# Kernel tuning notes

Hardware: AMD Instinct MI355X
Metric: run time of the kernel (lower is better)

## Reference

```python
import jax, jax.numpy as jnp
import numpy as np

V, L, D, C = 50000, 512, 300, 128
KS = (3, 4, 5)
B = 64


def setup_inputs() -> dict:
    key = jax.random.key(0)
    ks = jax.random.split(key, 12)
    inp = {
        "x": jax.random.randint(ks[0], (B, L), 0, V),
        "embed_w": jax.random.normal(ks[1], (V, D), jnp.float32) * 0.1,
        "conv_w": jax.random.normal(ks[2], (C, D), jnp.float32) * 0.05,
        "conv_b": jax.random.normal(ks[3], (C,), jnp.float32) * 0.05,
        "fc3_w": jax.random.normal(ks[4], (L - 3,), jnp.float32) * 0.04,
        "fc3_b": jax.random.normal(ks[5], (1,), jnp.float32) * 0.04,
        "fc4_w": jax.random.normal(ks[6], (L - 4,), jnp.float32) * 0.04,
        "fc4_b": jax.random.normal(ks[7], (1,), jnp.float32) * 0.04,
        "fc5_w": jax.random.normal(ks[8], (L - 5,), jnp.float32) * 0.04,
        "fc5_b": jax.random.normal(ks[9], (1,), jnp.float32) * 0.04,
        "fc_w": jax.random.normal(ks[10], (C, C * len(KS)), jnp.float32) * 0.05,
        "fc_b": jax.random.normal(ks[11], (C,), jnp.float32) * 0.05,
    }
    return inp


def reference(x, embed_w, conv_w, conv_b, fc3_w, fc3_b, fc4_w, fc4_b,
              fc5_w, fc5_b, fc_w, fc_b):
    # Embedding lookup: [B, L, D]
    emb = embed_w[x]
    # Exclusive prefix sum over the sequence dim (O(L) sliding sums).
    cs = jnp.concatenate(
        [jnp.zeros_like(emb[:, :1]), jnp.cumsum(emb, axis=1)], axis=1)  # [B, L+1, D]
    fcs = ((fc3_w, fc3_b), (fc4_w, fc4_b), (fc5_w, fc5_b))
    outs = []
    for k, (wk, bk) in zip(KS, fcs):
        # Window i sums tokens i..i+k-1; only L-k windows (range(L-k) in original).
        win = cs[:, k:L] - cs[:, :L - k]                      # [B, L-k, D]
        # conv_sim: dot each window-sum against C label vectors (kernel (1, D)).
        sim = jnp.einsum('bld,cd->bcl', win, conv_w) + conv_b[None, :, None]
        # Dropout is identity in eval; fcs[k]: Linear(L-k, 1) shared across channels.
        outs.append(jnp.einsum('bcl,l->bc', sim, wk) + bk)    # [B, C]
    h = jnp.concatenate(outs, axis=1)                          # [B, C*3]
    return h @ fc_w.T + fc_b                                   # [B, C]
```

## Files before the change

kernel.cpp:

```cpp
#include <hip/hip_runtime.h>
#include <stdint.h>

#define BB 64
#define LL 512
#define DD 300
#define CC 128

#define OFF_GRED (BB * 32 * 3 * DD)
#define OFF_HT   (OFF_GRED + BB * 3 * DD)
#define OFF_SKBK (OFF_HT + BB * 3 * CC)

__global__ __launch_bounds__(256) void k_gather(
    const int* __restrict__ x, const float* __restrict__ embed,
    const float* __restrict__ w3, const float* __restrict__ w4,
    const float* __restrict__ w5, float* __restrict__ Gpart) {
  const int b = blockIdx.x >> 4;
  const int tc = blockIdx.x & 15;
  const int tid = threadIdx.x;
  const int sub = tid >> 7;
  const int stid = tid & 127;

  __shared__ int sx[32];
  __shared__ float su[3][32];

  if (tid < 32) {
    const int t = tc * 32 + tid;
    sx[tid] = x[b * LL + t];
    const float* ws[3] = {w3, w4, w5};
#pragma unroll
    for (int kk = 0; kk < 3; ++kk) {
      const int k = kk + 3;
      int lo = t - k + 1; if (lo < 0) lo = 0;
      int hi = t; const int lim = LL - k - 1; if (hi > lim) hi = lim;
      float s = 0.f;
      for (int l = lo; l <= hi; ++l) s += ws[kk][l];
      su[kk][tid] = s;
    }
  }
  __syncthreads();

  float a0x = 0.f, a0y = 0.f, a1x = 0.f, a1y = 0.f, a2x = 0.f, a2y = 0.f;
  float c0x = 0.f, c0y = 0.f, c1x = 0.f, c1y = 0.f, c2x = 0.f, c2y = 0.f;
  const bool tail = stid < (DD / 2 - 128);

#pragma unroll
  for (int half = 0; half < 2; ++half) {
    const int base = sub * 16 + half * 8;
    float2 v[8], u[8];
#pragma unroll
    for (int i = 0; i < 8; ++i) {
      const float2* rp = (const float2*)(embed + (size_t)sx[base + i] * DD);
      v[i] = rp[stid];
    }
    if (tail) {
#pragma unroll
      for (int i = 0; i < 8; ++i) {
        const float2* rp = (const float2*)(embed + (size_t)sx[base + i] * DD);
        u[i] = rp[128 + stid];
      }
    }
#pragma unroll
    for (int i = 0; i < 8; ++i) {
      const int j = base + i;
      const float w0 = su[0][j], w1 = su[1][j], w2 = su[2][j];
      a0x += w0 * v[i].x; a0y += w0 * v[i].y;
      a1x += w1 * v[i].x; a1y += w1 * v[i].y;
      a2x += w2 * v[i].x; a2y += w2 * v[i].y;
      if (tail) {
        c0x += w0 * u[i].x; c0y += w0 * u[i].y;
        c1x += w1 * u[i].x; c1y += w1 * u[i].y;
        c2x += w2 * u[i].x; c2y += w2 * u[i].y;
      }
    }
  }

  const int p = tc * 2 + sub;
  float* Gp = Gpart + (size_t)(b * 32 + p) * (3 * DD);
  const int d0 = 2 * stid;
  Gp[0 * DD + d0] = a0x; Gp[0 * DD + d0 + 1] = a0y;
  Gp[1 * DD + d0] = a1x; Gp[1 * DD + d0 + 1] = a1y;
  Gp[2 * DD + d0] = a2x; Gp[2 * DD + d0 + 1] = a2y;
  if (tail) {
    const int d1 = 2 * (128 + stid);
    Gp[0 * DD + d1] = c0x; Gp[0 * DD + d1 + 1] = c0y;
    Gp[1 * DD + d1] = c1x; Gp[1 * DD + d1 + 1] = c1y;
    Gp[2 * DD + d1] = c2x; Gp[2 * DD + d1 + 1] = c2y;
  }
}

__global__ __launch_bounds__(256) void k_reduce(
    const float* __restrict__ Gpart,
    const float* __restrict__ w3, const float* __restrict__ b3,
    const float* __restrict__ w4, const float* __restrict__ b4,
    const float* __restrict__ w5, const float* __restrict__ b5,
    float* __restrict__ Gred, float* __restrict__ skbk) {
  const int blk = blockIdx.x;
  const int tid = threadIdx.x;

  if (blk < 225) {
    const int gid = blk * 256 + tid;
    const int out = gid >> 2;
    const int r = gid & 3;
    const int b = out / 225;
    const int q = out - b * 225;
    const float4* gp =
        (const float4*)Gpart + (size_t)b * 32 * 225 + (size_t)r * 8 * 225 + q;
    float4 s = gp[0];
#pragma unroll
    for (int p = 1; p < 8; ++p) {
      const float4 v = gp[(size_t)p * 225];
      s.x += v.x; s.y += v.y; s.z += v.z; s.w += v.w;
    }
#pragma unroll
    for (int off = 1; off <= 2; off <<= 1) {
      s.x += __shfl_down(s.x, off, 64);
      s.y += __shfl_down(s.y, off, 64);
      s.z += __shfl_down(s.z, off, 64);
      s.w += __shfl_down(s.w, off, 64);
    }
    if (r == 0) ((float4*)Gred)[out] = s;
  } else {
    __shared__ float red[256];
    const int kk = blk - 225;
    const float* wk = (kk == 0) ? w3 : ((kk == 1) ? w4 : w5);
    const float* bk = (kk == 0) ? b3 : ((kk == 1) ? b4 : b5);
    const int len = LL - (kk + 3);
    float s = (tid < len) ? wk[tid] : 0.f;
    if (tid + 256 < len) s += wk[tid + 256];
    red[tid] = s;
    __syncthreads();
    for (int off = 128; off >= 1; off >>= 1) {
      if (tid < off) red[tid] += red[tid + off];
      __syncthreads();
    }
    if (tid == 0) { skbk[kk] = red[0]; skbk[3 + kk] = bk[0]; }
  }
}

__global__ __launch_bounds__(256) void k_sim(
    const float* __restrict__ Gred, const float* __restrict__ conv_w,
    const float* __restrict__ conv_b, const float* __restrict__ skbk,
    float* __restrict__ hT) {
  const int o = blockIdx.x * 4 + (threadIdx.x >> 6);
  const int lane = threadIdx.x & 63;
  const int b = o / 384;
  const int j = o - b * 384;
  const int kk = j >> 7;
  const int cp = j & 127;

  const float2* cwp = (const float2*)(conv_w + cp * DD);
  const float2* g2 = (const float2*)(Gred + (b * 3 + kk) * DD);

  float acc;
  {
    const float2 v = cwp[lane];
    const float2 g = g2[lane];
    acc = v.x * g.x + v.y * g.y;
  }
  {
    const float2 v = cwp[lane + 64];
    const float2 g = g2[lane + 64];
    acc += v.x * g.x + v.y * g.y;
  }
  if (lane < 22) {
    const float2 v = cwp[lane + 128];
    const float2 g = g2[lane + 128];
    acc += v.x * g.x + v.y * g.y;
  }
#pragma unroll
  for (int off = 32; off >= 1; off >>= 1) acc += __shfl_down(acc, off, 64);
  if (lane == 0) {
    hT[b * (3 * CC) + j] = acc + conv_b[cp] * skbk[kk] + skbk[3 + kk];
  }
}

__global__ __launch_bounds__(256) void k_fc(
    const float* __restrict__ hT, const float* __restrict__ fcw,
    const float* __restrict__ fcb, float* __restrict__ out) {
  const int o = blockIdx.x * 4 + (threadIdx.x >> 6);
  const int lane = threadIdx.x & 63;
  const int b = o >> 7;
  const int c = o & 127;

  const float* fr = fcw + c * (3 * CC);
  const float* hr = hT + b * (3 * CC);
  float acc = 0.f;
#pragma unroll
  for (int s = 0; s < 6; ++s) acc += fr[s * 64 + lane] * hr[s * 64 + lane];
#pragma unroll
  for (int off = 32; off >= 1; off >>= 1) acc += __shfl_down(acc, off, 64);
  if (lane == 0) out[b * CC + c] = acc + fcb[c];
}

extern "C" void kernel_launch(void* const* d_in, const int* in_sizes, int n_in,
                              void* d_out, int out_size, void* d_ws,
                              size_t ws_size, hipStream_t stream) {
  const int* x = (const int*)d_in[0];
  const float* embed = (const float*)d_in[1];
  const float* conv_w = (const float*)d_in[2];
  const float* conv_b = (const float*)d_in[3];
  const float* fc3w = (const float*)d_in[4];
  const float* fc3b = (const float*)d_in[5];
  const float* fc4w = (const float*)d_in[6];
  const float* fc4b = (const float*)d_in[7];
  const float* fc5w = (const float*)d_in[8];
  const float* fc5b = (const float*)d_in[9];
  const float* fcw = (const float*)d_in[10];
  const float* fcb = (const float*)d_in[11];

  float* Gpart = (float*)d_ws;
  float* Gred = (float*)d_ws + OFF_GRED;
  float* hT = (float*)d_ws + OFF_HT;
  float* skbk = (float*)d_ws + OFF_SKBK;

  k_gather<<<dim3(BB * 16), dim3(256), 0, stream>>>(x, embed, fc3w, fc4w,
                                                    fc5w, Gpart);
  k_reduce<<<dim3(228), dim3(256), 0, stream>>>(Gpart, fc3w, fc3b, fc4w, fc4b,
                                                fc5w, fc5b, Gred, skbk);
  k_sim<<<dim3(6144), dim3(256), 0, stream>>>(Gred, conv_w, conv_b, skbk, hT);
  k_fc<<<dim3(2048), dim3(256), 0, stream>>>(hT, fcw, fcb, (float*)d_out);
}
```

Baseline: 129.7 us.

## Fuse partial-sum reduction and conv similarity into one kernel per batch-kernel pair

Merges the Gpart reduction, the fc weight-sum reduction and the conv_w dot-product stage into one kernel launched with one block per (batch, window size). Each block reduces its 32 partials into shared memory, computes the weight sum locally, and then loops over the 128 conv channels with one wavefront per 32 channels. This removes a kernel launch and the Gred/skbk global round trip. In exchange the grid drops to 192 blocks, and the weight-sum reduction is recomputed in every block.

```diff
diff --git a/kernel.cpp b/kernel.cpp
--- a/kernel.cpp
+++ b/kernel.cpp
@@ -6,9 +6,7 @@
 #define DD 300
 #define CC 128
 
-#define OFF_GRED (BB * 32 * 3 * DD)
-#define OFF_HT   (OFF_GRED + BB * 3 * DD)
-#define OFF_SKBK (OFF_HT + BB * 3 * CC)
+#define OFF_HT (BB * 32 * 3 * DD)
 
 __global__ __launch_bounds__(256) void k_gather(
     const int* __restrict__ x, const float* __restrict__ embed,
@@ -88,89 +86,91 @@
   }
 }
 
-__global__ __launch_bounds__(256) void k_reduce(
-    const float* __restrict__ Gpart,
+__global__ __launch_bounds__(256) void k_redsim(
+    const float* __restrict__ Gpart, const float* __restrict__ conv_w,
+    const float* __restrict__ conv_b,
     const float* __restrict__ w3, const float* __restrict__ b3,
     const float* __restrict__ w4, const float* __restrict__ b4,
     const float* __restrict__ w5, const float* __restrict__ b5,
-    float* __restrict__ Gred, float* __restrict__ skbk) {
+    float* __restrict__ hT) {
   const int blk = blockIdx.x;
+  const int b = blk / 3;
+  const int kk = blk - b * 3;
   const int tid = threadIdx.x;
-
-  if (blk < 225) {
-    const int gid = blk * 256 + tid;
-    const int out = gid >> 2;
-    const int r = gid & 3;
-    const int b = out / 225;
-    const int q = out - b * 225;
-    const float4* gp =
-        (const float4*)Gpart + (size_t)b * 32 * 225 + (size_t)r * 8 * 225 + q;
-    float4 s = gp[0];
-#pragma unroll
-    for (int p = 1; p < 8; ++p) {
-      const float4 v = gp[(size_t)p * 225];
-      s.x += v.x; s.y += v.y; s.z += v.z; s.w += v.w;
-    }
-#pragma unroll
-    for (int off = 1; off <= 2; off <<= 1) {
-      s.x += __shfl_down(s.x, off, 64);
-      s.y += __shfl_down(s.y, off, 64);
-      s.z += __shfl_down(s.z, off, 64);
-      s.w += __shfl_down(s.w, off, 64);
-    }
-    if (r == 0) ((float4*)Gred)[out] = s;
-  } else {
-    __shared__ float red[256];
-    const int kk = blk - 225;
-    const float* wk = (kk == 0) ? w3 : ((kk == 1) ? w4 : w5);
-    const float* bk = (kk == 0) ? b3 : ((kk == 1) ? b4 : b5);
+  const int sub = tid >> 7;
+  const int stid = tid & 127;
+
+  __shared__ float2 sGh[2][150];
+  __shared__ float red[256];
+
+  {
+    const float2* base =
+        (const float2*)Gpart + ((size_t)(b * 32 + sub * 16) * 3 + kk) * 150;
+    const bool tail = stid < 22;
+    float2 acc0 = {0.f, 0.f}, acc1 = {0.f, 0.f};
+#pragma unroll
+    for (int half = 0; half < 2; ++half) {
+      float2 v[8], u[8];
+#pragma unroll
+      for (int i = 0; i < 8; ++i)
+        v[i] = base[(size_t)(half * 8 + i) * 450 + stid];
+      if (tail) {
+#pragma unroll
+        for (int i = 0; i < 8; ++i)
+          u[i] = base[(size_t)(half * 8 + i) * 450 + 128 + stid];
+      }
+#pragma unroll
+      for (int i = 0; i < 8; ++i) {
+        acc0.x += v[i].x; acc0.y += v[i].y;
+        if (tail) { acc1.x += u[i].x; acc1.y += u[i].y; }
+      }
+    }
+    sGh[sub][stid] = acc0;
+    if (tail) sGh[sub][128 + stid] = acc1;
+  }
+
+  const float* wk = (kk == 0) ? w3 : ((kk == 1) ? w4 : w5);
+  const float* bk = (kk == 0) ? b3 : ((kk == 1) ? b4 : b5);
+  {
     const int len = LL - (kk + 3);
     float s = (tid < len) ? wk[tid] : 0.f;
     if (tid + 256 < len) s += wk[tid + 256];
     red[tid] = s;
+  }
+  __syncthreads();
+  for (int off = 128; off >= 1; off >>= 1) {
+    if (tid < off) red[tid] += red[tid + off];
     __syncthreads();
-    for (int off = 128; off >= 1; off >>= 1) {
-      if (tid < off) red[tid] += red[tid + off];
-      __syncthreads();
-    }
-    if (tid == 0) { skbk[kk] = red[0]; skbk[3 + kk] = bk[0]; }
-  }
-}
-
-__global__ __launch_bounds__(256) void k_sim(
-    const float* __restrict__ Gred, const float* __restrict__ conv_w,
-    const float* __restrict__ conv_b, const float* __restrict__ skbk,
-    float* __restrict__ hT) {
-  const int o = blockIdx.x * 4 + (threadIdx.x >> 6);
-  const int lane = threadIdx.x & 63;
-  const int b = o / 384;
-  const int j = o - b * 384;
-  const int kk = j >> 7;
-  const int cp = j & 127;
-
-  const float2* cwp = (const float2*)(conv_w + cp * DD);
-  const float2* g2 = (const float2*)(Gred + (b * 3 + kk) * DD);
-
-  float acc;
-  {
-    const float2 v = cwp[lane];
-    const float2 g = g2[lane];
-    acc = v.x * g.x + v.y * g.y;
-  }
-  {
-    const float2 v = cwp[lane + 64];
-    const float2 g = g2[lane + 64];
-    acc += v.x * g.x + v.y * g.y;
-  }
-  if (lane < 22) {
-    const float2 v = cwp[lane + 128];
-    const float2 g = g2[lane + 128];
-    acc += v.x * g.x + v.y * g.y;
-  }
-#pragma unroll
-  for (int off = 32; off >= 1; off >>= 1) acc += __shfl_down(acc, off, 64);
-  if (lane == 0) {
-    hT[b * (3 * CC) + j] = acc + conv_b[cp] * skbk[kk] + skbk[3 + kk];
+  }
+  const float Sk = red[0];
+  const float bkv = bk[0];
+
+  const int lane = tid & 63;
+  const int wid = tid >> 6;
+  for (int m = 0; m < 32; ++m) {
+    const int cp = wid * 32 + m;
+    const float2* cwp = (const float2*)(conv_w + cp * DD);
+    float acc;
+    {
+      const float2 v = cwp[lane];
+      const float2 g0 = sGh[0][lane], g1 = sGh[1][lane];
+      acc = v.x * (g0.x + g1.x) + v.y * (g0.y + g1.y);
+    }
+    {
+      const float2 v = cwp[lane + 64];
+      const float2 g0 = sGh[0][lane + 64], g1 = sGh[1][lane + 64];
+      acc += v.x * (g0.x + g1.x) + v.y * (g0.y + g1.y);
+    }
+    if (lane < 22) {
+      const float2 v = cwp[lane + 128];
+      const float2 g0 = sGh[0][lane + 128], g1 = sGh[1][lane + 128];
+      acc += v.x * (g0.x + g1.x) + v.y * (g0.y + g1.y);
+    }
+#pragma unroll
+    for (int off = 32; off >= 1; off >>= 1) acc += __shfl_down(acc, off, 64);
+    if (lane == 0) {
+      hT[b * (3 * CC) + kk * CC + cp] = acc + conv_b[cp] * Sk + bkv;
+    }
   }
 }
 
@@ -209,14 +209,11 @@
   const float* fcb = (const float*)d_in[11];
 
   float* Gpart = (float*)d_ws;
-  float* Gred = (float*)d_ws + OFF_GRED;
   float* hT = (float*)d_ws + OFF_HT;
-  float* skbk = (float*)d_ws + OFF_SKBK;
 
   k_gather<<<dim3(BB * 16), dim3(256), 0, stream>>>(x, embed, fc3w, fc4w,
                                                     fc5w, Gpart);
-  k_reduce<<<dim3(228), dim3(256), 0, stream>>>(Gpart, fc3w, fc3b, fc4w, fc4b,
-                                                fc5w, fc5b, Gred, skbk);
-  k_sim<<<dim3(6144), dim3(256), 0, stream>>>(Gred, conv_w, conv_b, skbk, hT);
+  k_redsim<<<dim3(BB * 3), dim3(256), 0, stream>>>(
+      Gpart, conv_w, conv_b, fc3w, fc3b, fc4w, fc4b, fc5w, fc5b, hT);
   k_fc<<<dim3(2048), dim3(256), 0, stream>>>(hT, fcw, fcb, (float*)d_out);
 }
```

Result: slower. 146.1 us (+12.6%).

## Fold conv weights into final FC weights and merge precompute into gather launch

Applied to the files above, without the earlier changes.

Precomputes W2 = fc_w·conv_w (per kernel size) and a combined bias inside extra blocks of the gather kernel, so the final stage becomes one dot product of length 900 per (batch, class). This removes the separate sim kernel and the intermediate hT buffer, cutting one launch and the 384-wide intermediate. The weight-product work is recomputed each call and runs alongside the gather blocks, which adds some extra compute to the first launch.

```diff
diff --git a/kernel.cpp b/kernel.cpp
--- a/kernel.cpp
+++ b/kernel.cpp
@@ -6,190 +6,193 @@
 #define DD 300
 #define CC 128
 
-#define OFF_GRED (BB * 32 * 3 * DD)
-#define OFF_HT   (OFF_GRED + BB * 3 * DD)
-#define OFF_SKBK (OFF_HT + BB * 3 * CC)
+#define OFF_GRED  (BB * 32 * 3 * DD)
+#define OFF_W2    (OFF_GRED + BB * 3 * DD)
+#define OFF_BIAS2 (OFF_W2 + CC * 3 * DD)
 
 __global__ __launch_bounds__(256) void k_gather(
     const int* __restrict__ x, const float* __restrict__ embed,
-    const float* __restrict__ w3, const float* __restrict__ w4,
-    const float* __restrict__ w5, float* __restrict__ Gpart) {
-  const int b = blockIdx.x >> 4;
-  const int tc = blockIdx.x & 15;
-  const int tid = threadIdx.x;
-  const int sub = tid >> 7;
-  const int stid = tid & 127;
-
-  __shared__ int sx[32];
-  __shared__ float su[3][32];
-
-  if (tid < 32) {
-    const int t = tc * 32 + tid;
-    sx[tid] = x[b * LL + t];
-    const float* ws[3] = {w3, w4, w5};
-#pragma unroll
-    for (int kk = 0; kk < 3; ++kk) {
-      const int k = kk + 3;
-      int lo = t - k + 1; if (lo < 0) lo = 0;
-      int hi = t; const int lim = LL - k - 1; if (hi > lim) hi = lim;
-      float s = 0.f;
-      for (int l = lo; l <= hi; ++l) s += ws[kk][l];
-      su[kk][tid] = s;
-    }
-  }
-  __syncthreads();
-
-  float a0x = 0.f, a0y = 0.f, a1x = 0.f, a1y = 0.f, a2x = 0.f, a2y = 0.f;
-  float c0x = 0.f, c0y = 0.f, c1x = 0.f, c1y = 0.f, c2x = 0.f, c2y = 0.f;
-  const bool tail = stid < (DD / 2 - 128);
-
-#pragma unroll
-  for (int half = 0; half < 2; ++half) {
-    const int base = sub * 16 + half * 8;
-    float2 v[8], u[8];
-#pragma unroll
-    for (int i = 0; i < 8; ++i) {
-      const float2* rp = (const float2*)(embed + (size_t)sx[base + i] * DD);
-      v[i] = rp[stid];
-    }
-    if (tail) {
-#pragma unroll
-      for (int i = 0; i < 8; ++i) {
-        const float2* rp = (const float2*)(embed + (size_t)sx[base + i] * DD);
-        u[i] = rp[128 + stid];
-      }
-    }
-#pragma unroll
-    for (int i = 0; i < 8; ++i) {
-      const int j = base + i;
-      const float w0 = su[0][j], w1 = su[1][j], w2 = su[2][j];
-      a0x += w0 * v[i].x; a0y += w0 * v[i].y;
-      a1x += w1 * v[i].x; a1y += w1 * v[i].y;
-      a2x += w2 * v[i].x; a2y += w2 * v[i].y;
-      if (tail) {
-        c0x += w0 * u[i].x; c0y += w0 * u[i].y;
-        c1x += w1 * u[i].x; c1y += w1 * u[i].y;
-        c2x += w2 * u[i].x; c2y += w2 * u[i].y;
-      }
-    }
-  }
-
-  const int p = tc * 2 + sub;
-  float* Gp = Gpart + (size_t)(b * 32 + p) * (3 * DD);
-  const int d0 = 2 * stid;
-  Gp[0 * DD + d0] = a0x; Gp[0 * DD + d0 + 1] = a0y;
-  Gp[1 * DD + d0] = a1x; Gp[1 * DD + d0 + 1] = a1y;
-  Gp[2 * DD + d0] = a2x; Gp[2 * DD + d0 + 1] = a2y;
-  if (tail) {
-    const int d1 = 2 * (128 + stid);
-    Gp[0 * DD + d1] = c0x; Gp[0 * DD + d1 + 1] = c0y;
-    Gp[1 * DD + d1] = c1x; Gp[1 * DD + d1 + 1] = c1y;
-    Gp[2 * DD + d1] = c2x; Gp[2 * DD + d1 + 1] = c2y;
-  }
-}
-
-__global__ __launch_bounds__(256) void k_reduce(
-    const float* __restrict__ Gpart,
+    const float* __restrict__ conv_w, const float* __restrict__ conv_b,
     const float* __restrict__ w3, const float* __restrict__ b3,
     const float* __restrict__ w4, const float* __restrict__ b4,
     const float* __restrict__ w5, const float* __restrict__ b5,
-    float* __restrict__ Gred, float* __restrict__ skbk) {
+    const float* __restrict__ fcw, const float* __restrict__ fcb,
+    float* __restrict__ Gpart, float* __restrict__ W2,
+    float* __restrict__ bias2) {
   const int blk = blockIdx.x;
   const int tid = threadIdx.x;
 
-  if (blk < 225) {
-    const int gid = blk * 256 + tid;
-    const int out = gid >> 2;
-    const int r = gid & 3;
-    const int b = out / 225;
-    const int q = out - b * 225;
-    const float4* gp =
-        (const float4*)Gpart + (size_t)b * 32 * 225 + (size_t)r * 8 * 225 + q;
-    float4 s = gp[0];
-#pragma unroll
-    for (int p = 1; p < 8; ++p) {
-      const float4 v = gp[(size_t)p * 225];
-      s.x += v.x; s.y += v.y; s.z += v.z; s.w += v.w;
-    }
-#pragma unroll
-    for (int off = 1; off <= 2; off <<= 1) {
-      s.x += __shfl_down(s.x, off, 64);
-      s.y += __shfl_down(s.y, off, 64);
-      s.z += __shfl_down(s.z, off, 64);
-      s.w += __shfl_down(s.w, off, 64);
-    }
-    if (r == 0) ((float4*)Gred)[out] = s;
+  if (blk < 1024) {
+    const int b = blk >> 4;
+    const int tc = blk & 15;
+    const int sub = tid >> 7;
+    const int stid = tid & 127;
+
+    __shared__ int sx[32];
+    __shared__ float su[3][32];
+
+    if (tid < 32) {
+      const int t = tc * 32 + tid;
+      sx[tid] = x[b * LL + t];
+      const float* ws[3] = {w3, w4, w5};
+#pragma unroll
+      for (int kk = 0; kk < 3; ++kk) {
+        const int k = kk + 3;
+        int lo = t - k + 1; if (lo < 0) lo = 0;
+        int hi = t; const int lim = LL - k - 1; if (hi > lim) hi = lim;
+        float s = 0.f;
+        for (int l = lo; l <= hi; ++l) s += ws[kk][l];
+        su[kk][tid] = s;
+      }
+    }
+    __syncthreads();
+
+    float a0x = 0.f, a0y = 0.f, a1x = 0.f, a1y = 0.f, a2x = 0.f, a2y = 0.f;
+    float c0x = 0.f, c0y = 0.f, c1x = 0.f, c1y = 0.f, c2x = 0.f, c2y = 0.f;
+    const bool tail = stid < (DD / 2 - 128);
+
+#pragma unroll
+    for (int half = 0; half < 2; ++half) {
+      const int base = sub * 16 + half * 8;
+      float2 v[8], u[8];
+#pragma unroll
+      for (int i = 0; i < 8; ++i) {
+        const float2* rp = (const float2*)(embed + (size_t)sx[base + i] * DD);
+        v[i] = rp[stid];
+      }
+      if (tail) {
+#pragma unroll
+        for (int i = 0; i < 8; ++i) {
+          const float2* rp =
+              (const float2*)(embed + (size_t)sx[base + i] * DD);
+          u[i] = rp[128 + stid];
+        }
+      }
+#pragma unroll
+      for (int i = 0; i < 8; ++i) {
+        const int j = base + i;
+        const float w0 = su[0][j], w1 = su[1][j], w2 = su[2][j];
+        a0x += w0 * v[i].x; a0y += w0 * v[i].y;
+        a1x += w1 * v[i].x; a1y += w1 * v[i].y;
+        a2x += w2 * v[i].x; a2y += w2 * v[i].y;
+        if (tail) {
+          c0x += w0 * u[i].x; c0y += w0 * u[i].y;
+          c1x += w1 * u[i].x; c1y += w1 * u[i].y;
+          c2x += w2 * u[i].x; c2y += w2 * u[i].y;
+        }
+      }
+    }
+
+    const int p = tc * 2 + sub;
+    float* Gp = Gpart + (size_t)(b * 32 + p) * (3 * DD);
+    const int d0 = 2 * stid;
+    Gp[0 * DD + d0] = a0x; Gp[0 * DD + d0 + 1] = a0y;
+    Gp[1 * DD + d0] = a1x; Gp[1 * DD + d0 + 1] = a1y;
+    Gp[2 * DD + d0] = a2x; Gp[2 * DD + d0 + 1] = a2y;
+    if (tail) {
+      const int d1 = 2 * (128 + stid);
+      Gp[0 * DD + d1] = c0x; Gp[0 * DD + d1 + 1] = c0y;
+      Gp[1 * DD + d1] = c1x; Gp[1 * DD + d1 + 1] = c1y;
+      Gp[2 * DD + d1] = c2x; Gp[2 * DD + d1 + 1] = c2y;
+    }
+  } else if (blk < 1504) {
+    const int w = (blk - 1024) * 4 + (tid >> 6);
+    const int lane = tid & 63;
+    const int c = w / 15;
+    const int rem = w - c * 15;
+    const int kk = rem / 5;
+    const int chunk = rem - kk * 5;
+    const int d = chunk * 64 + lane;
+    if (d < DD) {
+      const float* fr = fcw + c * (3 * CC) + kk * CC;
+      float acc0 = 0.f, acc1 = 0.f;
+#pragma unroll 4
+      for (int cp = 0; cp < CC; cp += 2) {
+        acc0 += fr[cp] * conv_w[cp * DD + d];
+        acc1 += fr[cp + 1] * conv_w[(cp + 1) * DD + d];
+      }
+      W2[c * (3 * DD) + kk * DD + d] = acc0 + acc1;
+    }
   } else {
-    __shared__ float red[256];
-    const int kk = blk - 225;
-    const float* wk = (kk == 0) ? w3 : ((kk == 1) ? w4 : w5);
-    const float* bk = (kk == 0) ? b3 : ((kk == 1) ? b4 : b5);
-    const int len = LL - (kk + 3);
-    float s = (tid < len) ? wk[tid] : 0.f;
-    if (tid + 256 < len) s += wk[tid + 256];
-    red[tid] = s;
-    __syncthreads();
-    for (int off = 128; off >= 1; off >>= 1) {
-      if (tid < off) red[tid] += red[tid + off];
-      __syncthreads();
-    }
-    if (tid == 0) { skbk[kk] = red[0]; skbk[3 + kk] = bk[0]; }
-  }
-}
-
-__global__ __launch_bounds__(256) void k_sim(
-    const float* __restrict__ Gred, const float* __restrict__ conv_w,
-    const float* __restrict__ conv_b, const float* __restrict__ skbk,
-    float* __restrict__ hT) {
-  const int o = blockIdx.x * 4 + (threadIdx.x >> 6);
-  const int lane = threadIdx.x & 63;
-  const int b = o / 384;
-  const int j = o - b * 384;
-  const int kk = j >> 7;
-  const int cp = j & 127;
-
-  const float2* cwp = (const float2*)(conv_w + cp * DD);
-  const float2* g2 = (const float2*)(Gred + (b * 3 + kk) * DD);
-
-  float acc;
-  {
-    const float2 v = cwp[lane];
-    const float2 g = g2[lane];
-    acc = v.x * g.x + v.y * g.y;
-  }
-  {
-    const float2 v = cwp[lane + 64];
-    const float2 g = g2[lane + 64];
-    acc += v.x * g.x + v.y * g.y;
-  }
-  if (lane < 22) {
-    const float2 v = cwp[lane + 128];
-    const float2 g = g2[lane + 128];
-    acc += v.x * g.x + v.y * g.y;
-  }
-#pragma unroll
-  for (int off = 32; off >= 1; off >>= 1) acc += __shfl_down(acc, off, 64);
-  if (lane == 0) {
-    hT[b * (3 * CC) + j] = acc + conv_b[cp] * skbk[kk] + skbk[3 + kk];
-  }
-}
-
-__global__ __launch_bounds__(256) void k_fc(
-    const float* __restrict__ hT, const float* __restrict__ fcw,
-    const float* __restrict__ fcb, float* __restrict__ out) {
+    const int wid = tid >> 6;
+    const int lane = tid & 63;
+    const int c = (blk - 1504) * 4 + wid;
+    float sk[3];
+    const float* ws[3] = {w3, w4, w5};
+#pragma unroll
+    for (int kk = 0; kk < 3; ++kk) {
+      const int len = LL - (kk + 3);
+      float s = 0.f;
+      for (int l = lane; l < len; l += 64) s += ws[kk][l];
+#pragma unroll
+      for (int off = 32; off >= 1; off >>= 1) s += __shfl_down(s, off, 64);
+      sk[kk] = __shfl(s, 0, 64);
+    }
+    const float bkv[3] = {b3[0], b4[0], b5[0]};
+    float acc = 0.f;
+#pragma unroll
+    for (int s6 = 0; s6 < 6; ++s6) {
+      const int j = s6 * 64 + lane;
+      const int kk = j >> 7;
+      const int cp = j & 127;
+      acc += fcw[c * (3 * CC) + j] * (conv_b[cp] * sk[kk] + bkv[kk]);
+    }
+#pragma unroll
+    for (int off = 32; off >= 1; off >>= 1) acc += __shfl_down(acc, off, 64);
+    if (lane == 0) bias2[c] = acc + fcb[c];
+  }
+}
+
+__global__ __launch_bounds__(256) void k_reduce(
+    const float* __restrict__ Gpart, float* __restrict__ Gred) {
+  const int gid = blockIdx.x * 256 + threadIdx.x;
+  const int out = gid >> 2;
+  const int r = gid & 3;
+  const int b = out / 225;
+  const int q = out - b * 225;
+  const float4* gp =
+      (const float4*)Gpart + (size_t)b * 32 * 225 + (size_t)r * 8 * 225 + q;
+  float4 s = gp[0];
+#pragma unroll
+  for (int p = 1; p < 8; ++p) {
+    const float4 v = gp[(size_t)p * 225];
+    s.x += v.x; s.y += v.y; s.z += v.z; s.w += v.w;
+  }
+#pragma unroll
+  for (int off = 1; off <= 2; off <<= 1) {
+    s.x += __shfl_down(s.x, off, 64);
+    s.y += __shfl_down(s.y, off, 64);
+    s.z += __shfl_down(s.z, off, 64);
+    s.w += __shfl_down(s.w, off, 64);
+  }
+  if (r == 0) ((float4*)Gred)[out] = s;
+}
+
+__global__ __launch_bounds__(256) void k_out(
+    const float* __restrict__ Gred, const float* __restrict__ W2,
+    const float* __restrict__ bias2, float* __restrict__ out) {
   const int o = blockIdx.x * 4 + (threadIdx.x >> 6);
   const int lane = threadIdx.x & 63;
   const int b = o >> 7;
   const int c = o & 127;
 
-  const float* fr = fcw + c * (3 * CC);
-  const float* hr = hT + b * (3 * CC);
+  const float2* wr = (const float2*)(W2 + c * (3 * DD));
+  const float2* gr = (const float2*)(Gred + b * (3 * DD));
   float acc = 0.f;
 #pragma unroll
-  for (int s = 0; s < 6; ++s) acc += fr[s * 64 + lane] * hr[s * 64 + lane];
+  for (int s = 0; s < 7; ++s) {
+    const float2 v = wr[s * 64 + lane];
+    const float2 g = gr[s * 64 + lane];
+    acc += v.x * g.x + v.y * g.y;
+  }
+  if (lane < 2) {
+    const float2 v = wr[448 + lane];
+    const float2 g = gr[448 + lane];
+    acc += v.x * g.x + v.y * g.y;
+  }
 #pragma unroll
   for (int off = 32; off >= 1; off >>= 1) acc += __shfl_down(acc, off, 64);
-  if (lane == 0) out[b * CC + c] = acc + fcb[c];
+  if (lane == 0) out[b * CC + c] = acc + bias2[c];
 }
 
 extern "C" void kernel_launch(void* const* d_in, const int* in_sizes, int n_in,
@@ -210,13 +213,13 @@
 
   float* Gpart = (float*)d_ws;
   float* Gred = (float*)d_ws + OFF_GRED;
-  float* hT = (float*)d_ws + OFF_HT;
-  float* skbk = (float*)d_ws + OFF_SKBK;
-
-  k_gather<<<dim3(BB * 16), dim3(256), 0, stream>>>(x, embed, fc3w, fc4w,
-                                                    fc5w, Gpart);
-  k_reduce<<<dim3(228), dim3(256), 0, stream>>>(Gpart, fc3w, fc3b, fc4w, fc4b,
-                                                fc5w, fc5b, Gred, skbk);
-  k_sim<<<dim3(6144), dim3(256), 0, stream>>>(Gred, conv_w, conv_b, skbk, hT);
-  k_fc<<<dim3(2048), dim3(256), 0, stream>>>(hT, fcw, fcb, (float*)d_out);
-}
+  float* W2 = (float*)d_ws + OFF_W2;
+  float* bias2 = (float*)d_ws + OFF_BIAS2;
+
+  k_gather<<<dim3(1536), dim3(256), 0, stream>>>(
+      x, embed, conv_w, conv_b, fc3w, fc3b, fc4w, fc4b, fc5w, fc5b, fcw, fcb,
+      Gpart, W2, bias2);
+  k_reduce<<<dim3(225), dim3(256), 0, stream>>>(Gpart, Gred);
+  k_out<<<dim3(2048), dim3(256), 0, stream>>>(Gred, W2, bias2,
+                                              (float*)d_out);
+}
```

After: 129.1 us. No clear change (-0.5%).
